# Performance work log

Hardware: AMD Instinct MI355X
Metric: run time of the kernel (lower is better)

## Reference

```python
import jax, jax.numpy as jnp
import numpy as np

WS = 7  # window_size


def _conv1x1(x, W, b):
    # 1x1 conv == channel-mixing matmul. W: [out_c, in_c], b: [out_c]
    return jnp.einsum('oc,bchw->bohw', W, x) + b[None, :, None, None]


def _window_flatten(t, ws):
    # [b, ch, H, W] -> [b, ch*nh*nw, ws*ws], matching torch unfold+contiguous+view
    b, ch, H, W = t.shape
    nh, nw = H // ws, W // ws
    t = t.reshape(b, ch, nh, ws, nw, ws).transpose(0, 1, 2, 4, 3, 5)  # [b,ch,nh,nw,ws,ws]
    return t.reshape(b, ch * nh * nw, ws * ws)


def setup_inputs() -> dict:
    key = jax.random.key(0)
    ks = jax.random.split(key, 7)
    b, c, h, w = 8, 256, 160, 160
    c8 = c // 8
    x = jax.random.normal(ks[0], (b, c, h, w), dtype=jnp.float32)
    Wq = jax.random.normal(ks[1], (c8, c), dtype=jnp.float32) * (1.0 / np.sqrt(c))
    bq = jnp.zeros((c8,), dtype=jnp.float32)
    Wk = jax.random.normal(ks[2], (c8, c), dtype=jnp.float32) * (1.0 / np.sqrt(c))
    bk = jnp.zeros((c8,), dtype=jnp.float32)
    Wv = jax.random.normal(ks[3], (c, c), dtype=jnp.float32) * (1.0 / np.sqrt(c))
    bv = jnp.zeros((c,), dtype=jnp.float32)
    return {"x": x, "Wq": Wq, "bq": bq, "Wk": Wk, "bk": bk, "Wv": Wv, "bv": bv}


def reference(x, Wq, bq, Wk, bk, Wv, bv):
    b, c, h, w = x.shape
    ws = WS
    pad_h = (ws - h % ws) % ws
    pad_w = (ws - w % ws) % ws
    xp = jnp.pad(x, ((0, 0), (0, 0), (0, pad_h), (0, pad_w)), mode='reflect')
    H, W = xp.shape[2], xp.shape[3]

    q = _window_flatten(_conv1x1(xp, Wq, bq), ws)  # [b, c8*nwin, 49]
    k = _window_flatten(_conv1x1(xp, Wk, bk), ws)  # [b, c8*nwin, 49]
    v = _window_flatten(_conv1x1(xp, Wv, bv), ws)  # [b, c*nwin, 49]

    # attn = softmax(q^T @ k) over last dim; reduction axis is channels*windows
    attn = jax.nn.softmax(jnp.einsum('bnp,bnq->bpq', q, k), axis=-1)  # [b,49,49]
    # out = v @ attn^T  -> out[b,m,i] = sum_j v[b,m,j] * attn[b,i,j]
    out = jnp.einsum('bmj,bij->bmi', v, attn)  # [b, c*nwin, 49]

    # faithful to torch .view(b, c, H, W) on contiguous [b,c,nh,nw,ws,ws] memory
    out = out.reshape(b, c, H, W)
    return out[:, :, :h, :w]
```

## Files before the change

kernel.cpp:

```cpp
#include <hip/hip_runtime.h>

#define C_ 256
#define HIN 160
#define NH 23
#define NWIN 529
#define G5 5
#define NGRP 106
#define OPLANE 25600

typedef short bf16x8 __attribute__((ext_vector_type(8)));
typedef float f32x4 __attribute__((ext_vector_type(4)));
typedef unsigned short u16x4 __attribute__((ext_vector_type(4)));

__device__ __forceinline__ unsigned short f2bf(float f) {
    union { float f; unsigned u; } v; v.f = f;
    unsigned r = v.u + 0x7FFFu + ((v.u >> 16) & 1u);
    return (unsigned short)(r >> 16);
}

__global__ void kprep(const float* __restrict__ Wq, const float* __restrict__ Wk,
                      const float* __restrict__ Wv, unsigned short* __restrict__ WvB,
                      float* __restrict__ W2t) {
    int t = blockIdx.x * 256 + threadIdx.x;
    if (t < 65536) WvB[t] = f2bf(Wv[t]);
    if (t < 16384) {
        int c = t >> 6, ch = t & 63;
        W2t[c * 64 + ch] = (ch < 32) ? Wq[ch * 256 + c] : Wk[(ch - 32) * 256 + c];
    }
}

#define QST 260
#define XST 264
__launch_bounds__(256, 2)
__global__ void k12(const float* __restrict__ x, const float* __restrict__ W2t,
                    const float* __restrict__ bq, const float* __restrict__ bk,
                    float* __restrict__ Spart) {
    __shared__ float QKs[64 * QST];
    __shared__ float Xs[8 * XST];
    __shared__ float Ws[8 * 64];

    int t = threadIdx.x;
    int g = blockIdx.x;
    int b = g & 7;
    int grp = g >> 3;
    int win0 = grp * G5;

    int wloc = t / 49, p = t % 49;
    int win = win0 + wloc;
    bool pxvalid = (t < 245) && (win < NWIN);
    const float* xp = x;
    if (pxvalid) {
        int wy = win / NH, wx = win % NH;
        int gy = wy * 7 + p / 7, gx = wx * 7 + p % 7;
        int sy = (gy < HIN) ? gy : 158;
        int sx = (gx < HIN) ? gx : 158;
        xp = x + (long)b * C_ * OPLANE + sy * HIN + sx;
    }

    int tx = t & 31, ty = t >> 5;

    float acc[8][8];
#pragma unroll
    for (int i = 0; i < 8; ++i)
#pragma unroll
        for (int j = 0; j < 8; ++j) acc[i][j] = 0.f;

    float prefX[8], prefW[2];
#pragma unroll
    for (int e = 0; e < 8; ++e) prefX[e] = pxvalid ? xp[(long)e * OPLANE] : 0.f;
#pragma unroll
    for (int i = 0; i < 2; ++i) {
        int idx = i * 256 + t, e = idx >> 6, ch = idx & 63;
        prefW[i] = W2t[e * 64 + ch];
    }

    for (int c0 = 0; c0 < 256; c0 += 8) {
#pragma unroll
        for (int e = 0; e < 8; ++e) Xs[e * XST + t] = prefX[e];
#pragma unroll
        for (int i = 0; i < 2; ++i) {
            int idx = i * 256 + t, e = idx >> 6, ch = idx & 63;
            Ws[e * 64 + ch] = prefW[i];
        }
        __syncthreads();
        if (c0 + 8 < 256) {
            int c1 = c0 + 8;
#pragma unroll
            for (int e = 0; e < 8; ++e) prefX[e] = pxvalid ? xp[(long)(c1 + e) * OPLANE] : 0.f;
#pragma unroll
            for (int i = 0; i < 2; ++i) {
                int idx = i * 256 + t, e = idx >> 6, ch = idx & 63;
                prefW[i] = W2t[(c1 + e) * 64 + ch];
            }
        }
#pragma unroll
        for (int kk = 0; kk < 8; ++kk) {
            float wv[8], xv[8];
#pragma unroll
            for (int i = 0; i < 8; ++i) wv[i] = Ws[kk * 64 + ty * 8 + i];
#pragma unroll
            for (int i = 0; i < 8; ++i) xv[i] = Xs[kk * XST + tx * 8 + i];
#pragma unroll
            for (int ci = 0; ci < 8; ++ci)
#pragma unroll
                for (int pi = 0; pi < 8; ++pi)
                    acc[ci][pi] = fmaf(wv[ci], xv[pi], acc[ci][pi]);
        }
        __syncthreads();
    }

    bool cvalid[8];
#pragma unroll
    for (int pi = 0; pi < 8; ++pi) {
        int px = tx * 8 + pi;
        int w = px / 49;
        cvalid[pi] = (px < 245) && (win0 + w < NWIN);
    }
    const float* bb = (ty < 4) ? (bq + ty * 8) : (bk + (ty - 4) * 8);
    float bias[8];
#pragma unroll
    for (int ci = 0; ci < 8; ++ci) bias[ci] = bb[ci];
#pragma unroll
    for (int ci = 0; ci < 8; ++ci) {
        int ch = ty * 8 + ci;
#pragma unroll
        for (int pi = 0; pi < 8; ++pi) {
            int px = tx * 8 + pi;
            QKs[ch * QST + px] = cvalid[pi] ? (acc[ci][pi] + bias[ci]) : 0.f;
        }
    }
    __syncthreads();

    if (t < 169) {
        int p0 = (t / 13) * 4, q0 = (t % 13) * 4;
        float s[4][4];
#pragma unroll
        for (int r = 0; r < 4; ++r)
#pragma unroll
            for (int cc = 0; cc < 4; ++cc) s[r][cc] = 0.f;
        for (int w = 0; w < G5; ++w) {
            for (int ch = 0; ch < 32; ++ch) {
                const float* qr = &QKs[ch * QST + w * 49 + p0];
                const float* kr = &QKs[(32 + ch) * QST + w * 49 + q0];
                float qv[4] = {qr[0], qr[1], qr[2], qr[3]};
                float kv[4] = {kr[0], kr[1], kr[2], kr[3]};
#pragma unroll
                for (int r = 0; r < 4; ++r)
#pragma unroll
                    for (int cc = 0; cc < 4; ++cc)
                        s[r][cc] = fmaf(qv[r], kv[cc], s[r][cc]);
            }
        }
        float* sp = Spart + (long)(b * NGRP + grp) * 2401;
#pragma unroll
        for (int r = 0; r < 4; ++r) {
            int pp = p0 + r;
            if (pp < 49) {
#pragma unroll
                for (int cc = 0; cc < 4; ++cc) {
                    int qq = q0 + cc;
                    if (qq < 49) sp[pp * 49 + qq] = s[r][cc];
                }
            }
        }
    }
}

__global__ void kred(const float* __restrict__ Spart, float* __restrict__ S) {
    int tg = blockIdx.x * 256 + threadIdx.x;
    if (tg >= 8 * 2401) return;
    int b = tg / 2401, idx = tg % 2401;
    float s = 0.f;
    for (int gr = 0; gr < NGRP; ++gr) s += Spart[(long)(b * NGRP + gr) * 2401 + idx];
    S[b * 2401 + idx] = s;
}

__global__ void ksoft(const float* __restrict__ S, unsigned short* __restrict__ attnP) {
    int b = blockIdx.x, t = threadIdx.x;
    unsigned short* row = attnP + (b * 64 + t) * 64;
    if (t < 49) {
        const float* sr = S + b * 2401 + t * 49;
        float m = -1e30f;
        for (int j = 0; j < 49; ++j) m = fmaxf(m, sr[j]);
        float den = 0.f;
        for (int j = 0; j < 49; ++j) den += expf(sr[j] - m);
        float inv = 1.f / den;
        for (int j = 0; j < 49; ++j) row[j] = f2bf(expf(sr[j] - m) * inv);
        for (int j = 49; j < 64; ++j) row[j] = 0;
    } else {
        for (int j = 0; j < 64; ++j) row[j] = 0;
    }
}

#define XCS 72
#define YTS 264
#define OTS 65
__launch_bounds__(256, 4)
__global__ void k3(const float* __restrict__ x, const unsigned short* __restrict__ WvB,
                   const unsigned short* __restrict__ attnP, const float* __restrict__ bv,
                   float* __restrict__ out) {
    __shared__ __align__(16) unsigned short U[256 * XCS];
    unsigned short* Xc = U;
    unsigned short* Yt = U;
    float* Ot = (float*)U;

    int t = threadIdx.x;
    int bw = blockIdx.x;
    int b = bw & 7;
    int win = bw >> 3;
    int wy = win / NH, wx = win % NH;
    int lane = t & 63;
    int r16 = lane & 15, quad = lane >> 4, q8 = quad * 8;
    int w64 = (t >> 6) * 64;

    const float* xb = x + (long)b * C_ * OPLANE;

    {
        int j = t & 63;
        bool jvalid = (j < 49);
        int gy = wy * 7 + j / 7, gx = wx * 7 + j % 7;
        int sy = (gy < HIN) ? gy : 158;
        int sx = (gx < HIN) ? gx : 158;
        const float* xs = xb + sy * HIN + sx;
#pragma unroll 4
        for (int c = (t >> 6); c < 256; c += 4) {
            float v = jvalid ? xs[(long)c * OPLANE] : 0.f;
            Xc[c * XCS + j] = f2bf(v);
        }
    }
    __syncthreads();

    f32x4 zero = {0.f, 0.f, 0.f, 0.f};
    f32x4 acc[4][4];
#pragma unroll
    for (int i = 0; i < 4; ++i)
#pragma unroll
        for (int j = 0; j < 4; ++j) acc[i][j] = zero;

#pragma unroll
    for (int half = 0; half < 2; ++half) {
        int k0 = half * 32;
        bf16x8 a[4], bfr[4];
#pragma unroll
        for (int mt = 0; mt < 4; ++mt)
            a[mt] = *(const bf16x8*)&Xc[(w64 + mt * 16 + r16) * XCS + k0 + q8];
#pragma unroll
        for (int nt = 0; nt < 4; ++nt)
            bfr[nt] = *(const bf16x8*)&attnP[(b * 64 + nt * 16 + r16) * 64 + k0 + q8];
#pragma unroll
        for (int mt = 0; mt < 4; ++mt)
#pragma unroll
            for (int nt = 0; nt < 4; ++nt)
                acc[mt][nt] = __builtin_amdgcn_mfma_f32_16x16x32_bf16(a[mt], bfr[nt], acc[mt][nt], 0, 0, 0);
    }
    __syncthreads();

#pragma unroll
    for (int mt = 0; mt < 4; ++mt) {
        int cb = w64 + mt * 16 + quad * 4;
#pragma unroll
        for (int nt = 0; nt < 4; ++nt) {
            int ic = nt * 16 + r16;
            u16x4 pk;
            pk[0] = f2bf(acc[mt][nt][0]);
            pk[1] = f2bf(acc[mt][nt][1]);
            pk[2] = f2bf(acc[mt][nt][2]);
            pk[3] = f2bf(acc[mt][nt][3]);
            *(u16x4*)&Yt[ic * YTS + cb] = pk;
        }
    }
    __syncthreads();

#pragma unroll
    for (int i = 0; i < 4; ++i)
#pragma unroll
        for (int j = 0; j < 4; ++j) acc[i][j] = zero;

#pragma unroll
    for (int ks = 0; ks < 8; ++ks) {
        int k0 = ks * 32;
        bf16x8 a[4], bb2[4];
#pragma unroll
        for (int mt = 0; mt < 4; ++mt)
            a[mt] = *(const bf16x8*)&WvB[(w64 + mt * 16 + r16) * 256 + k0 + q8];
#pragma unroll
        for (int nt = 0; nt < 4; ++nt)
            bb2[nt] = *(const bf16x8*)&Yt[(nt * 16 + r16) * YTS + k0 + q8];
#pragma unroll
        for (int mt = 0; mt < 4; ++mt)
#pragma unroll
            for (int nt = 0; nt < 4; ++nt)
                acc[mt][nt] = __builtin_amdgcn_mfma_f32_16x16x32_bf16(a[mt], bb2[nt], acc[mt][nt], 0, 0, 0);
    }
    __syncthreads();

    float* ob = out + (long)b * C_ * OPLANE;
    int f0 = win * 49;
    int y0 = f0 / 161, x0 = f0 - y0 * 161;
#pragma unroll
    for (int h = 0; h < 2; ++h) {
        if ((w64 >> 7) == h) {
#pragma unroll
            for (int mt = 0; mt < 4; ++mt) {
                int clb = (w64 & 127) + mt * 16 + quad * 4;
#pragma unroll
                for (int nt = 0; nt < 4; ++nt) {
                    int i = nt * 16 + r16;
                    if (i < 49) {
#pragma unroll
                        for (int r = 0; r < 4; ++r)
                            Ot[(clb + r) * OTS + i] = acc[mt][nt][r];
                    }
                }
            }
        }
        __syncthreads();
        for (int idx = t; idx < 128 * 49; idx += 256) {
            int cl = idx / 49;
            int jj = idx - cl * 49;
            int xx = x0 + jj, yy = y0;
            if (xx >= 161) { ++yy; xx -= 161; }
            if (xx < 160 && yy < 160) {
                int ch = h * 128 + cl;
                ob[ch * OPLANE + yy * 160 + xx] = Ot[cl * OTS + jj] + bv[ch];
            }
        }
        __syncthreads();
    }
}

extern "C" void kernel_launch(void* const* d_in, const int* in_sizes, int n_in,
                              void* d_out, int out_size, void* d_ws, size_t ws_size,
                              hipStream_t stream) {
    const float* x  = (const float*)d_in[0];
    const float* Wq = (const float*)d_in[1];
    const float* bq = (const float*)d_in[2];
    const float* Wk = (const float*)d_in[3];
    const float* bk = (const float*)d_in[4];
    const float* Wv = (const float*)d_in[5];
    const float* bv = (const float*)d_in[6];
    float* out = (float*)d_out;

    char* ws = (char*)d_ws;
    unsigned short* WvB   = (unsigned short*)(ws);
    float* W2t            = (float*)(ws + 131072);
    float* Spart          = (float*)(ws + 196608);
    float* S              = (float*)(ws + 196608 + 8144192);
    unsigned short* attnP = (unsigned short*)(ws + 196608 + 8144192 + 76832);

    kprep<<<dim3(256), dim3(256), 0, stream>>>(Wq, Wk, Wv, WvB, W2t);
    k12<<<dim3(8 * NGRP), dim3(256), 0, stream>>>(x, W2t, bq, bk, Spart);
    kred<<<dim3(76), dim3(256), 0, stream>>>(Spart, S);
    ksoft<<<dim3(8), dim3(64), 0, stream>>>(S, attnP);
    k3<<<dim3(8 * NWIN), dim3(256), 0, stream>>>(x, WvB, attnP, bv, out);
}
```

Before: 731.4 us.

## Use split-bf16 MFMA for QK projection, atomic reduction, and per-wave output staging

The fp32 FMA QK projection in k12 becomes MFMA, with x and the weights split into bf16 hi/lo parts (three MFMAs per tile) so fp32-level accuracy is kept. Windows per block go from 5 to 3. Per-group score partials are now summed with atomicAdd into a buffer that kprep zeroes, which removes the kred kernel and its partial-sum traffic. k3 gets batched x loads, setprio around the MFMA loops, and per-wave output staging that folds in the bias and drops block-wide barriers. The costs are more atomic traffic and a floating-point summation order that varies from run to run.

After: 606.1 us. 17.1% less time.

```diff
diff --git a/kernel.cpp b/kernel.cpp
--- a/kernel.cpp
+++ b/kernel.cpp
@@ -4,9 +4,13 @@
 #define HIN 160
 #define NH 23
 #define NWIN 529
-#define G5 5
-#define NGRP 106
 #define OPLANE 25600
+
+#define G3 3
+#define NG3 177
+#define NPX 160
+#define XSP 40
+#define QST2 164
 
 typedef short bf16x8 __attribute__((ext_vector_type(8)));
 typedef float f32x4 __attribute__((ext_vector_type(4)));
@@ -20,113 +24,121 @@
 
 __global__ void kprep(const float* __restrict__ Wq, const float* __restrict__ Wk,
                       const float* __restrict__ Wv, unsigned short* __restrict__ WvB,
-                      float* __restrict__ W2t) {
+                      unsigned short* __restrict__ W2h, unsigned short* __restrict__ W2l,
+                      float* __restrict__ S) {
     int t = blockIdx.x * 256 + threadIdx.x;
     if (t < 65536) WvB[t] = f2bf(Wv[t]);
     if (t < 16384) {
-        int c = t >> 6, ch = t & 63;
-        W2t[c * 64 + ch] = (ch < 32) ? Wq[ch * 256 + c] : Wk[(ch - 32) * 256 + c];
-    }
-}
-
-#define QST 260
-#define XST 264
+        int och = t >> 8, c = t & 255;
+        float w = (och < 32) ? Wq[och * 256 + c] : Wk[(och - 32) * 256 + c];
+        unsigned short h = f2bf(w);
+        union { unsigned u; float f; } uh; uh.u = (unsigned)h << 16;
+        W2h[t] = h;
+        W2l[t] = f2bf(w - uh.f);
+    }
+    if (t < 8 * 2401) S[t] = 0.f;
+}
+
 __launch_bounds__(256, 2)
-__global__ void k12(const float* __restrict__ x, const float* __restrict__ W2t,
-                    const float* __restrict__ bq, const float* __restrict__ bk,
-                    float* __restrict__ Spart) {
-    __shared__ float QKs[64 * QST];
-    __shared__ float Xs[8 * XST];
-    __shared__ float Ws[8 * 64];
+__global__ void k12(const float* __restrict__ x, const unsigned short* __restrict__ W2h,
+                    const unsigned short* __restrict__ W2l, const float* __restrict__ bq,
+                    const float* __restrict__ bk, float* __restrict__ S) {
+    __shared__ __align__(16) unsigned short Xh[NPX * XSP];
+    __shared__ __align__(16) unsigned short Xl[NPX * XSP];
+    __shared__ float QKs[64 * QST2];
 
     int t = threadIdx.x;
     int g = blockIdx.x;
-    int b = g & 7;
-    int grp = g >> 3;
-    int win0 = grp * G5;
-
-    int wloc = t / 49, p = t % 49;
-    int win = win0 + wloc;
-    bool pxvalid = (t < 245) && (win < NWIN);
-    const float* xp = x;
-    if (pxvalid) {
-        int wy = win / NH, wx = win % NH;
+    int b = g & 7, grp = g >> 3;
+    int win0 = grp * G3;
+    const float* xb = x + (long)b * C_ * OPLANE;
+
+    int c8 = t >> 5;
+    int j32 = t & 31;
+    const float* bases[5];
+    bool bval[5];
+#pragma unroll
+    for (int m = 0; m < 5; ++m) {
+        int px = j32 + 32 * m;
+        int w = px / 49, p = px - w * 49;
+        int win = win0 + w;
+        bool v = (px < 147) && (win < NWIN);
+        bval[m] = v;
+        int wy = win / NH, wx = win - wy * NH;
         int gy = wy * 7 + p / 7, gx = wx * 7 + p % 7;
         int sy = (gy < HIN) ? gy : 158;
         int sx = (gx < HIN) ? gx : 158;
-        xp = x + (long)b * C_ * OPLANE + sy * HIN + sx;
-    }
-
-    int tx = t & 31, ty = t >> 5;
-
-    float acc[8][8];
-#pragma unroll
-    for (int i = 0; i < 8; ++i)
-#pragma unroll
-        for (int j = 0; j < 8; ++j) acc[i][j] = 0.f;
-
-    float prefX[8], prefW[2];
-#pragma unroll
-    for (int e = 0; e < 8; ++e) prefX[e] = pxvalid ? xp[(long)e * OPLANE] : 0.f;
-#pragma unroll
-    for (int i = 0; i < 2; ++i) {
-        int idx = i * 256 + t, e = idx >> 6, ch = idx & 63;
-        prefW[i] = W2t[e * 64 + ch];
-    }
-
-    for (int c0 = 0; c0 < 256; c0 += 8) {
-#pragma unroll
-        for (int e = 0; e < 8; ++e) Xs[e * XST + t] = prefX[e];
-#pragma unroll
-        for (int i = 0; i < 2; ++i) {
-            int idx = i * 256 + t, e = idx >> 6, ch = idx & 63;
-            Ws[e * 64 + ch] = prefW[i];
+        bases[m] = v ? (xb + sy * HIN + sx) : xb;
+    }
+
+    int lane = t & 63, r16 = lane & 15, quad = lane >> 4, q8 = quad * 8;
+    int w = t >> 6;
+
+    f32x4 zero = {0.f, 0.f, 0.f, 0.f};
+    f32x4 acc[10];
+#pragma unroll
+    for (int nt = 0; nt < 10; ++nt) acc[nt] = zero;
+
+    float pf[20];
+#pragma unroll
+    for (int k = 0; k < 4; ++k)
+#pragma unroll
+        for (int m = 0; m < 5; ++m)
+            pf[k * 5 + m] = bval[m] ? bases[m][(long)(c8 + 8 * k) * OPLANE] : 0.f;
+
+    for (int c0 = 0; c0 < 256; c0 += 32) {
+#pragma unroll
+        for (int k = 0; k < 4; ++k) {
+            int cl = c8 + 8 * k;
+#pragma unroll
+            for (int m = 0; m < 5; ++m) {
+                int px = j32 + 32 * m;
+                float v = pf[k * 5 + m];
+                unsigned short h = f2bf(v);
+                union { unsigned u; float f; } uh; uh.u = (unsigned)h << 16;
+                Xh[px * XSP + cl] = h;
+                Xl[px * XSP + cl] = f2bf(v - uh.f);
+            }
         }
         __syncthreads();
-        if (c0 + 8 < 256) {
-            int c1 = c0 + 8;
-#pragma unroll
-            for (int e = 0; e < 8; ++e) prefX[e] = pxvalid ? xp[(long)(c1 + e) * OPLANE] : 0.f;
-#pragma unroll
-            for (int i = 0; i < 2; ++i) {
-                int idx = i * 256 + t, e = idx >> 6, ch = idx & 63;
-                prefW[i] = W2t[(c1 + e) * 64 + ch];
-            }
-        }
-#pragma unroll
-        for (int kk = 0; kk < 8; ++kk) {
-            float wv[8], xv[8];
-#pragma unroll
-            for (int i = 0; i < 8; ++i) wv[i] = Ws[kk * 64 + ty * 8 + i];
-#pragma unroll
-            for (int i = 0; i < 8; ++i) xv[i] = Xs[kk * XST + tx * 8 + i];
-#pragma unroll
-            for (int ci = 0; ci < 8; ++ci)
-#pragma unroll
-                for (int pi = 0; pi < 8; ++pi)
-                    acc[ci][pi] = fmaf(wv[ci], xv[pi], acc[ci][pi]);
-        }
+        if (c0 + 32 < 256) {
+            int c1 = c0 + 32;
+#pragma unroll
+            for (int k = 0; k < 4; ++k)
+#pragma unroll
+                for (int m = 0; m < 5; ++m)
+                    pf[k * 5 + m] = bval[m] ? bases[m][(long)(c1 + c8 + 8 * k) * OPLANE] : 0.f;
+        }
+        bf16x8 ah = *(const bf16x8*)&W2h[(16 * w + r16) * 256 + c0 + q8];
+        bf16x8 al = *(const bf16x8*)&W2l[(16 * w + r16) * 256 + c0 + q8];
+        __builtin_amdgcn_s_setprio(1);
+#pragma unroll
+        for (int nt = 0; nt < 10; ++nt) {
+            bf16x8 bh = *(const bf16x8*)&Xh[(nt * 16 + r16) * XSP + q8];
+            bf16x8 bl = *(const bf16x8*)&Xl[(nt * 16 + r16) * XSP + q8];
+            acc[nt] = __builtin_amdgcn_mfma_f32_16x16x32_bf16(ah, bh, acc[nt], 0, 0, 0);
+            acc[nt] = __builtin_amdgcn_mfma_f32_16x16x32_bf16(ah, bl, acc[nt], 0, 0, 0);
+            acc[nt] = __builtin_amdgcn_mfma_f32_16x16x32_bf16(al, bh, acc[nt], 0, 0, 0);
+        }
+        __builtin_amdgcn_s_setprio(0);
         __syncthreads();
     }
 
-    bool cvalid[8];
-#pragma unroll
-    for (int pi = 0; pi < 8; ++pi) {
-        int px = tx * 8 + pi;
-        int w = px / 49;
-        cvalid[pi] = (px < 245) && (win0 + w < NWIN);
-    }
-    const float* bb = (ty < 4) ? (bq + ty * 8) : (bk + (ty - 4) * 8);
-    float bias[8];
-#pragma unroll
-    for (int ci = 0; ci < 8; ++ci) bias[ci] = bb[ci];
-#pragma unroll
-    for (int ci = 0; ci < 8; ++ci) {
-        int ch = ty * 8 + ci;
-#pragma unroll
-        for (int pi = 0; pi < 8; ++pi) {
-            int px = tx * 8 + pi;
-            QKs[ch * QST + px] = cvalid[pi] ? (acc[ci][pi] + bias[ci]) : 0.f;
+    float bias[4];
+#pragma unroll
+    for (int r = 0; r < 4; ++r) {
+        int och = 16 * w + quad * 4 + r;
+        bias[r] = (och < 32) ? bq[och] : bk[och - 32];
+    }
+#pragma unroll
+    for (int nt = 0; nt < 10; ++nt) {
+        int px = nt * 16 + r16;
+        int wof = px / 49;
+        bool v = (px < 147) && (win0 + wof < NWIN);
+#pragma unroll
+        for (int r = 0; r < 4; ++r) {
+            int och = 16 * w + quad * 4 + r;
+            QKs[och * QST2 + px] = v ? (acc[nt][r] + bias[r]) : 0.f;
         }
     }
     __syncthreads();
@@ -138,10 +150,10 @@
         for (int r = 0; r < 4; ++r)
 #pragma unroll
             for (int cc = 0; cc < 4; ++cc) s[r][cc] = 0.f;
-        for (int w = 0; w < G5; ++w) {
+        for (int wi = 0; wi < G3; ++wi) {
             for (int ch = 0; ch < 32; ++ch) {
-                const float* qr = &QKs[ch * QST + w * 49 + p0];
-                const float* kr = &QKs[(32 + ch) * QST + w * 49 + q0];
+                const float* qr = &QKs[ch * QST2 + wi * 49 + p0];
+                const float* kr = &QKs[(32 + ch) * QST2 + wi * 49 + q0];
                 float qv[4] = {qr[0], qr[1], qr[2], qr[3]};
                 float kv[4] = {kr[0], kr[1], kr[2], kr[3]};
 #pragma unroll
@@ -151,7 +163,7 @@
                         s[r][cc] = fmaf(qv[r], kv[cc], s[r][cc]);
             }
         }
-        float* sp = Spart + (long)(b * NGRP + grp) * 2401;
+        float* sp = S + b * 2401;
 #pragma unroll
         for (int r = 0; r < 4; ++r) {
             int pp = p0 + r;
@@ -159,20 +171,11 @@
 #pragma unroll
                 for (int cc = 0; cc < 4; ++cc) {
                     int qq = q0 + cc;
-                    if (qq < 49) sp[pp * 49 + qq] = s[r][cc];
+                    if (qq < 49) atomicAdd(&sp[pp * 49 + qq], s[r][cc]);
                 }
             }
         }
     }
-}
-
-__global__ void kred(const float* __restrict__ Spart, float* __restrict__ S) {
-    int tg = blockIdx.x * 256 + threadIdx.x;
-    if (tg >= 8 * 2401) return;
-    int b = tg / 2401, idx = tg % 2401;
-    float s = 0.f;
-    for (int gr = 0; gr < NGRP; ++gr) s += Spart[(long)(b * NGRP + gr) * 2401 + idx];
-    S[b * 2401 + idx] = s;
 }
 
 __global__ void ksoft(const float* __restrict__ S, unsigned short* __restrict__ attnP) {
@@ -194,7 +197,7 @@
 
 #define XCS 72
 #define YTS 264
-#define OTS 65
+#define OTS2 50
 __launch_bounds__(256, 4)
 __global__ void k3(const float* __restrict__ x, const unsigned short* __restrict__ WvB,
                    const unsigned short* __restrict__ attnP, const float* __restrict__ bv,
@@ -202,7 +205,6 @@
     __shared__ __align__(16) unsigned short U[256 * XCS];
     unsigned short* Xc = U;
     unsigned short* Yt = U;
-    float* Ot = (float*)U;
 
     int t = threadIdx.x;
     int bw = blockIdx.x;
@@ -222,10 +224,16 @@
         int sy = (gy < HIN) ? gy : 158;
         int sx = (gx < HIN) ? gx : 158;
         const float* xs = xb + sy * HIN + sx;
-#pragma unroll 4
-        for (int c = (t >> 6); c < 256; c += 4) {
-            float v = jvalid ? xs[(long)c * OPLANE] : 0.f;
-            Xc[c * XCS + j] = f2bf(v);
+        int cb = t >> 6;
+#pragma unroll
+        for (int gg = 0; gg < 4; ++gg) {
+            float v[16];
+#pragma unroll
+            for (int i = 0; i < 16; ++i)
+                v[i] = jvalid ? xs[(long)(cb + 4 * (gg * 16 + i)) * OPLANE] : 0.f;
+#pragma unroll
+            for (int i = 0; i < 16; ++i)
+                Xc[(cb + 4 * (gg * 16 + i)) * XCS + j] = f2bf(v[i]);
         }
     }
     __syncthreads();
@@ -237,6 +245,7 @@
 #pragma unroll
         for (int j = 0; j < 4; ++j) acc[i][j] = zero;
 
+    __builtin_amdgcn_s_setprio(1);
 #pragma unroll
     for (int half = 0; half < 2; ++half) {
         int k0 = half * 32;
@@ -253,6 +262,7 @@
             for (int nt = 0; nt < 4; ++nt)
                 acc[mt][nt] = __builtin_amdgcn_mfma_f32_16x16x32_bf16(a[mt], bfr[nt], acc[mt][nt], 0, 0, 0);
     }
+    __builtin_amdgcn_s_setprio(0);
     __syncthreads();
 
 #pragma unroll
@@ -276,6 +286,7 @@
 #pragma unroll
         for (int j = 0; j < 4; ++j) acc[i][j] = zero;
 
+    __builtin_amdgcn_s_setprio(1);
 #pragma unroll
     for (int ks = 0; ks < 8; ++ks) {
         int k0 = ks * 32;
@@ -292,40 +303,42 @@
             for (int nt = 0; nt < 4; ++nt)
                 acc[mt][nt] = __builtin_amdgcn_mfma_f32_16x16x32_bf16(a[mt], bb2[nt], acc[mt][nt], 0, 0, 0);
     }
-    __syncthreads();
-
+    __builtin_amdgcn_s_setprio(0);
+    __syncthreads();
+
+    float* Os = (float*)U + (t >> 6) * (32 * OTS2);
     float* ob = out + (long)b * C_ * OPLANE;
     int f0 = win * 49;
     int y0 = f0 / 161, x0 = f0 - y0 * 161;
 #pragma unroll
-    for (int h = 0; h < 2; ++h) {
-        if ((w64 >> 7) == h) {
-#pragma unroll
-            for (int mt = 0; mt < 4; ++mt) {
-                int clb = (w64 & 127) + mt * 16 + quad * 4;
-#pragma unroll
-                for (int nt = 0; nt < 4; ++nt) {
-                    int i = nt * 16 + r16;
-                    if (i < 49) {
-#pragma unroll
-                        for (int r = 0; r < 4; ++r)
-                            Ot[(clb + r) * OTS + i] = acc[mt][nt][r];
-                    }
+    for (int sub = 0; sub < 2; ++sub) {
+#pragma unroll
+        for (int mt2 = 0; mt2 < 2; ++mt2) {
+            int mt = sub * 2 + mt2;
+            int clb = mt2 * 16 + quad * 4;
+            int chb = w64 + mt * 16 + quad * 4;
+            float bvl[4];
+#pragma unroll
+            for (int r = 0; r < 4; ++r) bvl[r] = bv[chb + r];
+#pragma unroll
+            for (int nt = 0; nt < 4; ++nt) {
+                int i = nt * 16 + r16;
+                if (i < 49) {
+#pragma unroll
+                    for (int r = 0; r < 4; ++r)
+                        Os[(clb + r) * OTS2 + i] = acc[mt][nt][r] + bvl[r];
                 }
             }
         }
-        __syncthreads();
-        for (int idx = t; idx < 128 * 49; idx += 256) {
-            int cl = idx / 49;
-            int jj = idx - cl * 49;
+        for (int idx = lane; idx < 32 * 49; idx += 64) {
+            int cl = idx / 49, jj = idx - cl * 49;
             int xx = x0 + jj, yy = y0;
             if (xx >= 161) { ++yy; xx -= 161; }
             if (xx < 160 && yy < 160) {
-                int ch = h * 128 + cl;
-                ob[ch * OPLANE + yy * 160 + xx] = Ot[cl * OTS + jj] + bv[ch];
-            }
-        }
-        __syncthreads();
+                int ch = w64 + sub * 32 + cl;
+                ob[ch * OPLANE + yy * 160 + xx] = Os[cl * OTS2 + jj];
+            }
+        }
     }
 }
 
@@ -343,14 +356,13 @@
 
     char* ws = (char*)d_ws;
     unsigned short* WvB   = (unsigned short*)(ws);
-    float* W2t            = (float*)(ws + 131072);
-    float* Spart          = (float*)(ws + 196608);
-    float* S              = (float*)(ws + 196608 + 8144192);
-    unsigned short* attnP = (unsigned short*)(ws + 196608 + 8144192 + 76832);
-
-    kprep<<<dim3(256), dim3(256), 0, stream>>>(Wq, Wk, Wv, WvB, W2t);
-    k12<<<dim3(8 * NGRP), dim3(256), 0, stream>>>(x, W2t, bq, bk, Spart);
-    kred<<<dim3(76), dim3(256), 0, stream>>>(Spart, S);
+    unsigned short* W2h   = (unsigned short*)(ws + 131072);
+    unsigned short* W2l   = (unsigned short*)(ws + 163840);
+    float* S              = (float*)(ws + 196608);
+    unsigned short* attnP = (unsigned short*)(ws + 273440);
+
+    kprep<<<dim3(256), dim3(256), 0, stream>>>(Wq, Wk, Wv, WvB, W2h, W2l, S);
+    k12<<<dim3(8 * NG3), dim3(256), 0, stream>>>(x, W2h, W2l, bq, bk, S);
     ksoft<<<dim3(8), dim3(64), 0, stream>>>(S, attnP);
     k3<<<dim3(8 * NWIN), dim3(256), 0, stream>>>(x, WvB, attnP, bv, out);
 }
```
